# Optimization experiments

Measured on AMD Instinct MI355X. Metric: run time of the kernel, lower is better.

Reference implementation:

```python
import jax, jax.numpy as jnp
import numpy as np
from jax import lax

B, N, C = 8, 3136, 512
NUM_HEADS = 8
HEAD_DIM = C // NUM_HEADS
KS = 5  # depthwise conv kernel size


def setup_inputs() -> dict:
    key = jax.random.key(0)
    ks = jax.random.split(key, 8)
    s = 0.02
    return {
        "x": jax.random.normal(ks[0], (B, N, C), dtype=jnp.float32),
        "H": 56,
        "W": 56,
        "Wq": jax.random.normal(ks[1], (C, C), dtype=jnp.float32) * s,
        "Wkv": jax.random.normal(ks[2], (C, 2 * C), dtype=jnp.float32) * s,
        "pos_enc": jnp.zeros((1, N, C), dtype=jnp.float32),
        "dwc_w": jax.random.normal(ks[3], (HEAD_DIM, 1, KS, KS), dtype=jnp.float32) * s,
        "dwc_b": jnp.zeros((HEAD_DIM,), dtype=jnp.float32),
        "Wproj": jax.random.normal(ks[4], (C, C), dtype=jnp.float32) * s,
        "bproj": jnp.zeros((C,), dtype=jnp.float32),
    }


def _split_heads(t):
    # (B, N, C) -> (B*h, N, head_dim), matching 'b n (h c) -> (b h) n c'
    b, n, c = t.shape
    return t.reshape(b, n, NUM_HEADS, HEAD_DIM).transpose(0, 2, 1, 3).reshape(b * NUM_HEADS, n, HEAD_DIM)


def reference(x, H, W, Wq, Wkv, pos_enc, dwc_w, dwc_b, Wproj, bproj):
    b, n, c = x.shape
    # projections (qkv_bias=False)
    q = jnp.maximum(x @ Wq, 0.0)                       # ReLU kernel feature map
    kv = x @ Wkv
    k = jnp.maximum(kv[..., :c] + pos_enc, 0.0)
    v = kv[..., c:]

    q = _split_heads(q)  # (bh, n, d)
    k = _split_heads(k)
    v = _split_heads(v)

    # normalizer z_i = 1 / (q_i . sum_j k_j + eps)
    z = 1.0 / (jnp.einsum('bic,bc->bi', q, k.sum(axis=1)) + 1e-6)
    # kv-first ordering (i*j*(c+d) > c*d*(i+j) for these shapes)
    kvmat = jnp.einsum('bjc,bjd->bcd', k, v)           # (bh, d, d)
    out = jnp.einsum('bic,bcd->bid', q, kvmat) * z[..., None]

    # depthwise conv residual on v: 'b (w h) c -> b c w h'
    num = int(round(n ** 0.5))
    fmap = v.reshape(-1, num, num, HEAD_DIM).transpose(0, 3, 1, 2)  # (bh, d, num, num)
    fmap = lax.conv_general_dilated(
        fmap, dwc_w, window_strides=(1, 1), padding='SAME',
        feature_group_count=HEAD_DIM,
        dimension_numbers=('NCHW', 'OIHW', 'NCHW'))
    fmap = fmap + dwc_b[None, :, None, None]
    fmap = fmap.transpose(0, 2, 3, 1).reshape(-1, n, HEAD_DIM)
    out = out + fmap

    # merge heads: '(b h) n c -> b n (h c)'
    out = out.reshape(b, NUM_HEADS, n, HEAD_DIM).transpose(0, 2, 1, 3).reshape(b, n, c)
    return out @ Wproj + bproj
```

## Files before the change

kernel.cpp:

```cpp
#include <hip/hip_runtime.h>
#include <stdint.h>

#define B_    8
#define N_    3136
#define C_    512
#define MTOT  25088

typedef __attribute__((ext_vector_type(8))) short bf16x8;
typedef __attribute__((ext_vector_type(4))) float f32x4;

__device__ __forceinline__ float bf2f(short s){
  union { float f; uint32_t u; } cv; cv.u = ((uint32_t)(uint16_t)s) << 16; return cv.f;
}
__device__ __forceinline__ short f2bf(float f){
  union { float f; uint32_t u; } cv; cv.f = f;
  uint32_t r = cv.u + 0x7FFFu + ((cv.u >> 16) & 1u);
  return (short)(r >> 16);
}

typedef const __attribute__((address_space(1))) void* gas1_t;
typedef __attribute__((address_space(3))) void* las3_t;
__device__ __forceinline__ void gld16(const void* g, void* l){
  __builtin_amdgcn_global_load_lds((gas1_t)g, (las3_t)l, 16, 0, 0);
}

#define BARR  __builtin_amdgcn_s_barrier()
#define SCHB  __builtin_amdgcn_sched_barrier(0)
#define VMC0  asm volatile("s_waitcnt vmcnt(0)" ::: "memory")
#define VMC4  asm volatile("s_waitcnt vmcnt(4)" ::: "memory")
#define VMC6  asm volatile("s_waitcnt vmcnt(6)" ::: "memory")
#define LGKM0  asm volatile("s_waitcnt lgkmcnt(0)" ::: "memory")
#define LGKM2  asm volatile("s_waitcnt lgkmcnt(2)" ::: "memory")
#define LGKM10 asm volatile("s_waitcnt lgkmcnt(10)" ::: "memory")

__global__ __launch_bounds__(256) void cvt_x(const float* __restrict__ x,
                                             short* __restrict__ xb, int n8){
  int i = blockIdx.x * 256 + threadIdx.x;
  if (i >= n8) return;
  const float4* p = (const float4*)x;
  float4 a = p[i*2], b = p[i*2+1];
  short o[8] = { f2bf(a.x), f2bf(a.y), f2bf(a.z), f2bf(a.w),
                 f2bf(b.x), f2bf(b.y), f2bf(b.z), f2bf(b.w) };
  *(bf16x8*)(xb + i*8) = *(bf16x8*)o;
}

__global__ __launch_bounds__(256) void tconv(const float* __restrict__ src,
                                             short* __restrict__ dst, int J){
  __shared__ float tile[32][33];
  int jb = blockIdx.x * 32, kb = blockIdx.y * 32;
  int tx = threadIdx.x & 31, ty = threadIdx.x >> 5;
#pragma unroll
  for (int r = 0; r < 32; r += 8)
    tile[ty + r][tx] = src[(size_t)(kb + ty + r) * J + jb + tx];
  __syncthreads();
#pragma unroll
  for (int r = 0; r < 32; r += 8)
    dst[(size_t)(jb + ty + r) * 512 + kb + tx] = f2bf(tile[tx][ty + r]);
}

__global__ __launch_bounds__(256) void conv_wT(const float* __restrict__ w,
                                               float* __restrict__ wt){
  int i = blockIdx.x * 256 + threadIdx.x;
  if (i < 1600) { int c = i / 25, tap = i - c * 25; wt[tap * 64 + c] = w[i]; }
}

template<int MODE, int NCT>
__global__ __launch_bounds__(512, 2)
void gemm_bf16(const short* __restrict__ A, const short* __restrict__ Bt,
               short* __restrict__ oQ, short* __restrict__ oK, short* __restrict__ oV,
               const float* __restrict__ posenc,
               float* __restrict__ oF, const float* __restrict__ bias)
{
  extern __shared__ __align__(16) char lds[];
  const int tid = threadIdx.x;
  const int wave = tid >> 6, lane = tid & 63;
  const int fr = lane & 15;

  constexpr int nwg = 98 * NCT;
  constexpr int q8 = nwg / 8, r8 = nwg % 8;
  const int orig = blockIdx.x;
  const int xcd = orig & 7, lid = orig >> 3;
  const int swz = (xcd < r8 ? xcd * (q8 + 1) : r8 * (q8 + 1) + (xcd - r8) * q8) + lid;
  const int rt = (swz / NCT) * 256;
  const int ct = (swz % NCT) * 256;

  const int wm = (wave >> 2) * 128;
  const int wn = (wave & 3) * 64;

  const int srow = lane >> 2;
  const int csrc = ((lane & 3) ^ ((lane >> 3) & 3)) << 3;
  const short* srcA = A  + (size_t)(rt + wave * 32 + srow) * 512 + csrc;
  const short* srcB = Bt + (size_t)(ct + wave * 32 + srow) * 512 + csrc;
  char* dA = lds + wave * 2048;
  char* dB = lds + 32768 + wave * 2048;

  auto stage = [&](int sbb, int isB, int ks, int tt) {
    const short* s = (isB ? srcB : srcA) + tt * 64 + ks * 32;
    char* d = (isB ? dB : dA) + sbb + ks * 16384;
    gld16(s,        d);
    gld16(s + 8192, d + 1024);
  };

  const int cR   = (((lane >> 4) ^ ((fr >> 1) & 3)) << 4);
  const int offA = (wm + fr) * 64 + cR;
  const int offB = 32768 + (wn + fr) * 64 + cR;

#define READ_A(dst, bufb, ks) do { \
    const char* _p = lds + (bufb) + (ks) * 16384 + offA; \
    _Pragma("unroll") \
    for (int _i = 0; _i < 8; _i++) dst[_i] = *(const bf16x8*)(_p + _i * 1024); \
  } while (0)
#define READ_B2(dst, bufb, ks, j0) do { \
    const char* _p = lds + (bufb) + (ks) * 16384 + offB + (j0) * 1024; \
    dst[0] = *(const bf16x8*)(_p); \
    dst[1] = *(const bf16x8*)(_p + 1024); \
  } while (0)
#define MFMA16(afv, bv, jb) do { \
    __builtin_amdgcn_s_setprio(1); \
    _Pragma("unroll") \
    for (int _i = 0; _i < 8; _i++) { \
      acc[_i][jb]     = __builtin_amdgcn_mfma_f32_16x16x32_bf16(afv[_i], bv[0], acc[_i][jb],     0, 0, 0); \
      acc[_i][jb + 1] = __builtin_amdgcn_mfma_f32_16x16x32_bf16(afv[_i], bv[1], acc[_i][jb + 1], 0, 0, 0); \
    } \
    __builtin_amdgcn_s_setprio(0); \
  } while (0)

  f32x4 zv = {0.f, 0.f, 0.f, 0.f};
  f32x4 acc[8][4];
#pragma unroll
  for (int i = 0; i < 8; i++)
#pragma unroll
    for (int j = 0; j < 4; j++) acc[i][j] = zv;

  bf16x8 afU[8], afV[8], bX[2], bY[2];

  stage(0, 0, 0, 0); stage(0, 1, 0, 0); stage(0, 0, 1, 0); stage(0, 1, 1, 0);
  VMC4; BARR; SCHB;
  READ_A(afU, 0, 0);
  READ_B2(bX, 0, 0, 0);

  for (int t = 0; t < 7; ++t) {
    const int bufb = (t & 1) * 65536, sbb = bufb ^ 65536;
    stage(sbb, 0, 0, t + 1);
    VMC6; BARR; SCHB;
    READ_B2(bY, bufb, 0, 2);
    LGKM2; SCHB;
    MFMA16(afU, bX, 0);
    stage(sbb, 1, 0, t + 1);
    VMC4; BARR; SCHB;
    READ_A(afV, bufb, 1);
    READ_B2(bX, bufb, 1, 0);
    LGKM10; SCHB;
    MFMA16(afU, bY, 2);
    stage(sbb, 0, 1, t + 1);
    VMC6; BARR; SCHB;
    READ_B2(bY, bufb, 1, 2);
    LGKM2; SCHB;
    MFMA16(afV, bX, 0);
    stage(sbb, 1, 1, t + 1);
    VMC4; BARR; SCHB;
    READ_A(afU, sbb, 0);
    READ_B2(bX, sbb, 0, 0);
    LGKM10; SCHB;
    MFMA16(afV, bY, 2);
  }
  {
    const int bufb = 65536;
    VMC4; BARR; SCHB;
    READ_B2(bY, bufb, 0, 2);
    LGKM2; SCHB;
    MFMA16(afU, bX, 0);
    VMC0; BARR; SCHB;
    READ_A(afV, bufb, 1);
    READ_B2(bX, bufb, 1, 0);
    LGKM10; SCHB;
    MFMA16(afU, bY, 2);
    READ_B2(bY, bufb, 1, 2);
    LGKM2; SCHB;
    MFMA16(afV, bX, 0);
    LGKM0; SCHB;
    MFMA16(afV, bY, 2);
  }

  BARR; SCHB;

  const int rb = (lane >> 4) << 2;
  if (MODE == 0) {
    short* ov = (short*)lds;
    const int sel = ct >> 9;
    const int cb  = ct - sel * 512;
    short* outp = sel == 0 ? oQ : (sel == 1 ? oK : oV);
#pragma unroll
    for (int q4 = 0; q4 < 4; ++q4) {
      if (q4) __syncthreads();
      if ((wave >> 2) == (q4 >> 1)) {
        const int ib = (q4 & 1) * 4;
#pragma unroll
        for (int ii = 0; ii < 4; ii++)
#pragma unroll
          for (int j = 0; j < 4; j++)
#pragma unroll
            for (int r = 0; r < 4; r++)
              ov[(ii * 16 + rb + r) * 260 + wn + j * 16 + fr] = f2bf(acc[ib + ii][j][r]);
      }
      __syncthreads();
#pragma unroll
      for (int p = 0; p < 4; ++p) {
        int id = tid + 512 * p;
        int row = id >> 5, cc = (id & 31) * 8;
        bf16x8 vv = *(const bf16x8*)&ov[row * 260 + cc];
        int grow = rt + q4 * 64 + row;
        short o[8];
        if (sel == 0) {
#pragma unroll
          for (int e = 0; e < 8; e++) o[e] = f2bf(fmaxf(bf2f(vv[e]), 0.f));
        } else if (sel == 1) {
          int nr = grow % N_;
          const float* pp = posenc + (size_t)nr * 512 + cb + cc;
          f32x4 p0 = *(const f32x4*)pp;
          f32x4 p1 = *(const f32x4*)(pp + 4);
#pragma unroll
          for (int e = 0; e < 4; e++) {
            o[e]     = f2bf(fmaxf(bf2f(vv[e]) + p0[e], 0.f));
            o[e + 4] = f2bf(fmaxf(bf2f(vv[e + 4]) + p1[e], 0.f));
          }
        } else {
#pragma unroll
          for (int e = 0; e < 8; e++) o[e] = vv[e];
        }
        *(bf16x8*)(outp + (size_t)grow * 512 + cb + cc) = *(bf16x8*)o;
      }
    }
  } else {
    float* ovf = (float*)lds;
#pragma unroll
    for (int q4 = 0; q4 < 4; ++q4) {
      if (q4) __syncthreads();
      if ((wave >> 2) == (q4 >> 1)) {
        const int ib = (q4 & 1) * 4;
#pragma unroll
        for (int ii = 0; ii < 4; ii++)
#pragma unroll
          for (int j = 0; j < 4; j++)
#pragma unroll
            for (int r = 0; r < 4; r++)
              ovf[(ii * 16 + rb + r) * 260 + wn + j * 16 + fr] = acc[ib + ii][j][r];
      }
      __syncthreads();
#pragma unroll
      for (int p = 0; p < 4; ++p) {
        int id = tid + 512 * p;
        int row = id >> 5, cc = (id & 31) * 8;
        f32x4 v0 = *(const f32x4*)&ovf[row * 260 + cc];
        f32x4 v1 = *(const f32x4*)&ovf[row * 260 + cc + 4];
        v0 += *(const f32x4*)&bias[ct + cc];
        v1 += *(const f32x4*)&bias[ct + cc + 4];
        float* op = oF + (size_t)(rt + q4 * 64 + row) * 512 + ct + cc;
        *(f32x4*)op       = v0;
        *(f32x4*)(op + 4) = v1;
      }
    }
  }
#undef READ_A
#undef READ_B2
#undef MFMA16
}

__global__ __launch_bounds__(256)
void kvmat_part(const short* __restrict__ kb, const short* __restrict__ vb,
                float* __restrict__ pKV, float* __restrict__ pKS)
{
  __shared__ __align__(16) float lk[64][64];
  __shared__ __align__(16) float lv[64][64];
  const int chunk = blockIdx.x, bh = blockIdx.y;
  const int b = bh >> 3, h = bh & 7;
  const int t = threadIdx.x;
  const int tc = t >> 4, td = t & 15;
  const int kc = t & 63, kr = (t >> 6) * 16;
  float acc[4][4] = {};
  float ksacc = 0.f;

  for (int tile = 0; tile < 7; ++tile) {
    const int r0 = chunk * 448 + tile * 64;
    __syncthreads();
#pragma unroll
    for (int i = 0; i < 2; i++) {
      int idx = t + i * 256;
      int r = idx >> 3, c8 = (idx & 7) << 3;
      size_t g = (size_t)(b * N_ + r0 + r) * 512 + h * 64 + c8;
      bf16x8 kk = *(const bf16x8*)(kb + g);
      bf16x8 vv = *(const bf16x8*)(vb + g);
#pragma unroll
      for (int e = 0; e < 8; e++) { lk[r][c8 + e] = bf2f(kk[e]); lv[r][c8 + e] = bf2f(vv[e]); }
    }
    __syncthreads();
#pragma unroll 4
    for (int r = 0; r < 64; r++) {
      f32x4 k4 = *(const f32x4*)&lk[r][tc * 4];
      f32x4 v4 = *(const f32x4*)&lv[r][td * 4];
#pragma unroll
      for (int i = 0; i < 4; i++)
#pragma unroll
        for (int j = 0; j < 4; j++) acc[i][j] += k4[i] * v4[j];
    }
#pragma unroll 4
    for (int rr = 0; rr < 16; rr++) ksacc += lk[kr + rr][kc];
  }

  const int pbase = (bh * 7 + chunk) * 4096;
#pragma unroll
  for (int i = 0; i < 4; i++)
#pragma unroll
    for (int j = 0; j < 4; j++)
      pKV[pbase + (tc * 4 + i) * 64 + td * 4 + j] = acc[i][j];
  __syncthreads();
  float* red = &lk[0][0];
  red[t] = ksacc;
  __syncthreads();
  if (t < 64)
    pKS[(bh * 7 + chunk) * 64 + t] = red[t] + red[t + 64] + red[t + 128] + red[t + 192];
}

__global__ __launch_bounds__(256)
void kv_reduce(const float* __restrict__ pKV, const float* __restrict__ pKS,
               short* __restrict__ kvT, float* __restrict__ ksum)
{
  int bh = blockIdx.x, t = threadIdx.x;
#pragma unroll
  for (int i = 0; i < 16; i++) {
    int idx = t + i * 256;
    float s = 0.f;
#pragma unroll
    for (int c = 0; c < 7; c++) s += pKV[(bh * 7 + c) * 4096 + idx];
    int cc = idx >> 6, d = idx & 63;
    kvT[bh * 4096 + d * 64 + cc] = f2bf(s);
  }
  if (t < 64) {
    float s = 0.f;
#pragma unroll
    for (int c = 0; c < 7; c++) s += pKS[(bh * 7 + c) * 64 + t];
    ksum[bh * 64 + t] = s;
  }
}

__global__ __launch_bounds__(256)
void conv_dw(const short* __restrict__ vb, const float* __restrict__ wT,
             const float* __restrict__ bias, short* __restrict__ pre)
{
  __shared__ __align__(16) short lsv[5 * 56 * 64];
  __shared__ __align__(16) float lwT[25 * 64];
  const int y = blockIdx.x, bh = blockIdx.y;
  const int b = bh >> 3, h = bh & 7;
  const int t = threadIdx.x;
  for (int i = t; i < 1600; i += 256) lwT[i] = wT[i];
  for (int i = t; i < 2240; i += 256) {
    int row = i / 448, rem = i - row * 448;
    int xx = rem >> 3, c8i = rem & 7;
    int gy = y + row - 2;
    bf16x8 val = {0, 0, 0, 0, 0, 0, 0, 0};
    if ((unsigned)gy < 56u)
      val = *(const bf16x8*)(vb + (size_t)(b * N_ + gy * 56 + xx) * 512 + h * 64 + c8i * 8);
    *(bf16x8*)(lsv + i * 8) = val;
  }
  __syncthreads();

  const int c8 = t & 7;
  const int x0 = t >> 3;
  float acc0[8], acc1[8];
  {
    f32x4 b0 = *(const f32x4*)&bias[c8 * 8];
    f32x4 b1 = *(const f32x4*)&bias[c8 * 8 + 4];
#pragma unroll
    for (int e = 0; e < 4; e++) { acc0[e] = b0[e]; acc0[e+4] = b1[e];
                                  acc1[e] = b0[e]; acc1[e+4] = b1[e]; }
  }
#pragma unroll
  for (int dy = 0; dy < 5; ++dy) {
#pragma unroll
    for (int dx = 0; dx < 5; ++dx) {
      float w8[8];
      {
        const float* wp = &lwT[(dy * 5 + dx) * 64 + c8 * 8];
        *(f32x4*)&w8[0] = *(const f32x4*)wp;
        *(f32x4*)&w8[4] = *(const f32x4*)(wp + 4);
      }
      const int base = dy * 56 * 64 + c8 * 8;
      int xxa = x0 + dx - 2;
      if ((unsigned)xxa < 56u) {
        bf16x8 v = *(const bf16x8*)(lsv + base + xxa * 64);
#pragma unroll
        for (int e = 0; e < 8; e++) acc0[e] += bf2f(v[e]) * w8[e];
      }
      int xxb = xxa + 32;
      if (xxb < 56) {
        bf16x8 v = *(const bf16x8*)(lsv + base + xxb * 64);
#pragma unroll
        for (int e = 0; e < 8; e++) acc1[e] += bf2f(v[e]) * w8[e];
      }
    }
  }
  size_t gbase = (size_t)(b * N_ + y * 56 + x0) * 512 + h * 64 + c8 * 8;
  short o[8];
#pragma unroll
  for (int e = 0; e < 8; e++) o[e] = f2bf(acc0[e]);
  *(bf16x8*)(pre + gbase) = *(bf16x8*)o;
  if (x0 + 32 < 56) {
#pragma unroll
    for (int e = 0; e < 8; e++) o[e] = f2bf(acc1[e]);
    *(bf16x8*)(pre + gbase + (size_t)32 * 512) = *(bf16x8*)o;
  }
}

__global__ __launch_bounds__(64)
void attn_mfma(const short* __restrict__ qb, const short* __restrict__ kvT,
               const float* __restrict__ ksum, short* __restrict__ pre)
{
  __shared__ __align__(16) float ov[64 * 68];
  __shared__ float lks[64];
  const int pt = blockIdx.x, bh = blockIdx.y;
  const int b = bh >> 3, h = bh & 7;
  const int l = threadIdx.x;
  const int fr = l & 15, kg = l >> 4;
  const int n0 = pt * 64;

  lks[l] = ksum[bh * 64 + l];

  const short* qbase = qb + (size_t)(b * N_ + n0) * 512 + h * 64;
  const short* kvb   = kvT + bh * 4096;
  bf16x8 af[4][2], bm[4][2];
#pragma unroll
  for (int i = 0; i < 4; i++)
#pragma unroll
    for (int s = 0; s < 2; s++) {
      af[i][s] = *(const bf16x8*)(qbase + (size_t)(fr + i * 16) * 512 + s * 32 + kg * 8);
      bm[i][s] = *(const bf16x8*)(kvb + (fr + i * 16) * 64 + s * 32 + kg * 8);
    }

  f32x4 zv4 = {0.f, 0.f, 0.f, 0.f};
  f32x4 acc[4][4];
#pragma unroll
  for (int i = 0; i < 4; i++)
#pragma unroll
    for (int j = 0; j < 4; j++) acc[i][j] = zv4;
#pragma unroll
  for (int s = 0; s < 2; s++)
#pragma unroll
    for (int i = 0; i < 4; i++)
#pragma unroll
      for (int j = 0; j < 4; j++)
        acc[i][j] = __builtin_amdgcn_mfma_f32_16x16x32_bf16(af[i][s], bm[j][s], acc[i][j], 0, 0, 0);

  const short* qrow = qb + (size_t)(b * N_ + n0 + l) * 512 + h * 64;
  float zd = 0.f;
#pragma unroll
  for (int g = 0; g < 8; g++) {
    bf16x8 qv = *(const bf16x8*)(qrow + g * 8);
#pragma unroll
    for (int e = 0; e < 8; e++) zd += bf2f(qv[e]) * lks[g * 8 + e];
  }
  const float z = 1.f / (zd + 1e-6f);

  const int rb = kg << 2;
#pragma unroll
  for (int i = 0; i < 4; i++)
#pragma unroll
    for (int j = 0; j < 4; j++)
#pragma unroll
      for (int r = 0; r < 4; r++)
        ov[(i * 16 + rb + r) * 68 + j * 16 + fr] = acc[i][j][r];
  __syncthreads();

  size_t gb = (size_t)(b * N_ + n0 + l) * 512 + h * 64;
  const float* ovr = &ov[l * 68];
#pragma unroll
  for (int g = 0; g < 8; g++) {
    bf16x8 pv = *(const bf16x8*)(pre + gb + g * 8);
    f32x4 a0 = *(const f32x4*)(ovr + g * 8);
    f32x4 a1 = *(const f32x4*)(ovr + g * 8 + 4);
    short o[8];
#pragma unroll
    for (int e = 0; e < 4; e++) {
      o[e]     = f2bf(a0[e] * z + bf2f(pv[e]));
      o[e + 4] = f2bf(a1[e] * z + bf2f(pv[e + 4]));
    }
    *(bf16x8*)(pre + gb + g * 8) = *(bf16x8*)o;
  }
}

extern "C" void kernel_launch(void* const* d_in, const int* in_sizes, int n_in,
                              void* d_out, int out_size, void* d_ws, size_t ws_size,
                              hipStream_t stream)
{
  const float* x     = (const float*)d_in[0];
  const float* Wq    = (const float*)d_in[3];
  const float* Wkv   = (const float*)d_in[4];
  const float* pos   = (const float*)d_in[5];
  const float* dwcw  = (const float*)d_in[6];
  const float* dwcb  = (const float*)d_in[7];
  const float* Wproj = (const float*)d_in[8];
  const float* bproj = (const float*)d_in[9];
  float* out = (float*)d_out;

  char* ws = (char*)d_ws;
  size_t off = 0;
  auto alloc = [&](size_t bytes) -> void* {
    void* p = ws + off;
    off = (off + bytes + 255) & ~(size_t)255;
    return p;
  };
  short* xb     = (short*)alloc((size_t)MTOT * 512 * 2);
  short* wqkvT  = (short*)alloc((size_t)1536 * 512 * 2);
  short* wprojT = (short*)alloc((size_t)512 * 512 * 2);
  float* wTc    = (float*)alloc((size_t)25 * 64 * 4);
  short* qb     = (short*)alloc((size_t)MTOT * 512 * 2);
  short* kbuf   = (short*)alloc((size_t)MTOT * 512 * 2);
  short* vbuf   = (short*)alloc((size_t)MTOT * 512 * 2);
  float* pKV    = (float*)alloc((size_t)64 * 7 * 4096 * 4);
  float* pKS    = (float*)alloc((size_t)64 * 7 * 64 * 4);
  short* kvT    = (short*)alloc((size_t)64 * 4096 * 2);
  float* ksumB  = (float*)alloc((size_t)64 * 64 * 4);
  short* pre    = (short*)alloc((size_t)MTOT * 512 * 2);
  if (ws_size < off) return;

  {
    auto k0 = gemm_bf16<0, 6>;
    auto k1 = gemm_bf16<1, 2>;
    hipFuncSetAttribute(reinterpret_cast<const void*>(k0),
                        hipFuncAttributeMaxDynamicSharedMemorySize, 131072);
    hipFuncSetAttribute(reinterpret_cast<const void*>(k1),
                        hipFuncAttributeMaxDynamicSharedMemorySize, 131072);
  }

  cvt_x<<<dim3((MTOT * 512 / 8 + 255) / 256), dim3(256), 0, stream>>>(x, xb, MTOT * 512 / 8);
  conv_wT<<<dim3(7), dim3(256), 0, stream>>>(dwcw, wTc);
  tconv<<<dim3(16, 16), dim3(256), 0, stream>>>(Wq,    wqkvT,              512);
  tconv<<<dim3(32, 16), dim3(256), 0, stream>>>(Wkv,   wqkvT + 512 * 512, 1024);
  tconv<<<dim3(16, 16), dim3(256), 0, stream>>>(Wproj, wprojT,             512);
  gemm_bf16<0, 6><<<dim3(588), dim3(512), 131072, stream>>>(xb, wqkvT, qb, kbuf, vbuf, pos,
                                                            nullptr, nullptr);
  kvmat_part<<<dim3(7, 64), dim3(256), 0, stream>>>(kbuf, vbuf, pKV, pKS);
  kv_reduce<<<dim3(64), dim3(256), 0, stream>>>(pKV, pKS, kvT, ksumB);
  conv_dw<<<dim3(56, 64), dim3(256), 0, stream>>>(vbuf, wTc, dwcb, pre);
  attn_mfma<<<dim3(49, 64), dim3(64), 0, stream>>>(qb, kvT, ksumB, pre);
  gemm_bf16<1, 2><<<dim3(196), dim3(512), 131072, stream>>>(pre, wprojT, nullptr, nullptr, nullptr,
                                                            nullptr, out, bproj);
}
```

Measured before the change: 220.5 us.

## Shrink GEMM tiles and use a three-stage LDS pipeline for higher occupancy

Rewrites the bf16 GEMM mainloop to use 128-row tiles (128x256 for the QKV projection, 128x128 for the output projection) with a simple three-buffer, K-step-of-32 pipeline in place of the hand-scheduled double-buffered 256x256 loop. LDS usage and register footprint drop so launch bounds rise to 4 blocks per CU, and the grids quadruple or double. The epilogue becomes a single LDS staging pass. The aim is more workgroups to fill the CUs and more latency hiding from occupancy. The cost is lower per-block data reuse, more global traffic for the operands, and the loss of the interleaved LDS-read/MFMA scheduling.

```diff
diff --git a/kernel.cpp b/kernel.cpp
--- a/kernel.cpp
+++ b/kernel.cpp
@@ -27,11 +27,9 @@
 #define BARR  __builtin_amdgcn_s_barrier()
 #define SCHB  __builtin_amdgcn_sched_barrier(0)
 #define VMC0  asm volatile("s_waitcnt vmcnt(0)" ::: "memory")
-#define VMC4  asm volatile("s_waitcnt vmcnt(4)" ::: "memory")
-#define VMC6  asm volatile("s_waitcnt vmcnt(6)" ::: "memory")
-#define LGKM0  asm volatile("s_waitcnt lgkmcnt(0)" ::: "memory")
-#define LGKM2  asm volatile("s_waitcnt lgkmcnt(2)" ::: "memory")
-#define LGKM10 asm volatile("s_waitcnt lgkmcnt(10)" ::: "memory")
+#define VMC2  asm volatile("s_waitcnt vmcnt(2)" ::: "memory")
+#define VMC3  asm volatile("s_waitcnt vmcnt(3)" ::: "memory")
+#define LGKM0 asm volatile("s_waitcnt lgkmcnt(0)" ::: "memory")
 
 __global__ __launch_bounds__(256) void cvt_x(const float* __restrict__ x,
                                              short* __restrict__ xb, int n8){
@@ -65,121 +63,82 @@
 }
 
 template<int MODE, int NCT>
-__global__ __launch_bounds__(512, 2)
+__global__ __launch_bounds__(512, 4)
 void gemm_bf16(const short* __restrict__ A, const short* __restrict__ Bt,
                short* __restrict__ oQ, short* __restrict__ oK, short* __restrict__ oV,
                const float* __restrict__ posenc,
                float* __restrict__ oF, const float* __restrict__ bias)
 {
+  constexpr int BN    = MODE ? 128 : 256;
+  constexpr int NJ    = MODE ? 2 : 4;
+  constexpr int WNW   = MODE ? 32 : 64;
+  constexpr int BUFSZ = MODE ? 16384 : 24576;
+  constexpr int BOFF  = 8192;
   extern __shared__ __align__(16) char lds[];
   const int tid = threadIdx.x;
   const int wave = tid >> 6, lane = tid & 63;
   const int fr = lane & 15;
 
-  constexpr int nwg = 98 * NCT;
+  constexpr int nwg = 196 * NCT;
   constexpr int q8 = nwg / 8, r8 = nwg % 8;
   const int orig = blockIdx.x;
   const int xcd = orig & 7, lid = orig >> 3;
   const int swz = (xcd < r8 ? xcd * (q8 + 1) : r8 * (q8 + 1) + (xcd - r8) * q8) + lid;
-  const int rt = (swz / NCT) * 256;
-  const int ct = (swz % NCT) * 256;
-
-  const int wm = (wave >> 2) * 128;
-  const int wn = (wave & 3) * 64;
+  const int rt = (swz / NCT) * 128;
+  const int ct = (swz % NCT) * BN;
+
+  const int wm = (wave >> 2) * 64;
+  const int wn = (wave & 3) * WNW;
 
   const int srow = lane >> 2;
   const int csrc = ((lane & 3) ^ ((lane >> 3) & 3)) << 3;
-  const short* srcA = A  + (size_t)(rt + wave * 32 + srow) * 512 + csrc;
-  const short* srcB = Bt + (size_t)(ct + wave * 32 + srow) * 512 + csrc;
-  char* dA = lds + wave * 2048;
-  char* dB = lds + 32768 + wave * 2048;
-
-  auto stage = [&](int sbb, int isB, int ks, int tt) {
-    const short* s = (isB ? srcB : srcA) + tt * 64 + ks * 32;
-    char* d = (isB ? dB : dA) + sbb + ks * 16384;
-    gld16(s,        d);
-    gld16(s + 8192, d + 1024);
+  const short* srcA = A  + (size_t)(rt + wave * 16 + srow) * 512 + csrc;
+  const short* srcB = Bt + (size_t)(ct + wave * (MODE ? 16 : 32) + srow) * 512 + csrc;
+  char* dA = lds + wave * 1024;
+  char* dB = lds + BOFF + wave * (MODE ? 1024 : 2048);
+
+  auto stage = [&](int t) {
+    const int b = (t % 3) * BUFSZ;
+    const short* a0 = srcA + t * 32;
+    gld16(a0, dA + b);
+    const short* b0 = srcB + t * 32;
+    gld16(b0, dB + b);
+    if (MODE == 0) gld16(b0 + 8192, dB + b + 1024);
   };
 
   const int cR   = (((lane >> 4) ^ ((fr >> 1) & 3)) << 4);
   const int offA = (wm + fr) * 64 + cR;
-  const int offB = 32768 + (wn + fr) * 64 + cR;
-
-#define READ_A(dst, bufb, ks) do { \
-    const char* _p = lds + (bufb) + (ks) * 16384 + offA; \
-    _Pragma("unroll") \
-    for (int _i = 0; _i < 8; _i++) dst[_i] = *(const bf16x8*)(_p + _i * 1024); \
-  } while (0)
-#define READ_B2(dst, bufb, ks, j0) do { \
-    const char* _p = lds + (bufb) + (ks) * 16384 + offB + (j0) * 1024; \
-    dst[0] = *(const bf16x8*)(_p); \
-    dst[1] = *(const bf16x8*)(_p + 1024); \
-  } while (0)
-#define MFMA16(afv, bv, jb) do { \
-    __builtin_amdgcn_s_setprio(1); \
-    _Pragma("unroll") \
-    for (int _i = 0; _i < 8; _i++) { \
-      acc[_i][jb]     = __builtin_amdgcn_mfma_f32_16x16x32_bf16(afv[_i], bv[0], acc[_i][jb],     0, 0, 0); \
-      acc[_i][jb + 1] = __builtin_amdgcn_mfma_f32_16x16x32_bf16(afv[_i], bv[1], acc[_i][jb + 1], 0, 0, 0); \
-    } \
-    __builtin_amdgcn_s_setprio(0); \
-  } while (0)
+  const int offB = BOFF + (wn + fr) * 64 + cR;
 
   f32x4 zv = {0.f, 0.f, 0.f, 0.f};
-  f32x4 acc[8][4];
-#pragma unroll
-  for (int i = 0; i < 8; i++)
-#pragma unroll
-    for (int j = 0; j < 4; j++) acc[i][j] = zv;
-
-  bf16x8 afU[8], afV[8], bX[2], bY[2];
-
-  stage(0, 0, 0, 0); stage(0, 1, 0, 0); stage(0, 0, 1, 0); stage(0, 1, 1, 0);
-  VMC4; BARR; SCHB;
-  READ_A(afU, 0, 0);
-  READ_B2(bX, 0, 0, 0);
-
-  for (int t = 0; t < 7; ++t) {
-    const int bufb = (t & 1) * 65536, sbb = bufb ^ 65536;
-    stage(sbb, 0, 0, t + 1);
-    VMC6; BARR; SCHB;
-    READ_B2(bY, bufb, 0, 2);
-    LGKM2; SCHB;
-    MFMA16(afU, bX, 0);
-    stage(sbb, 1, 0, t + 1);
-    VMC4; BARR; SCHB;
-    READ_A(afV, bufb, 1);
-    READ_B2(bX, bufb, 1, 0);
-    LGKM10; SCHB;
-    MFMA16(afU, bY, 2);
-    stage(sbb, 0, 1, t + 1);
-    VMC6; BARR; SCHB;
-    READ_B2(bY, bufb, 1, 2);
-    LGKM2; SCHB;
-    MFMA16(afV, bX, 0);
-    stage(sbb, 1, 1, t + 1);
-    VMC4; BARR; SCHB;
-    READ_A(afU, sbb, 0);
-    READ_B2(bX, sbb, 0, 0);
-    LGKM10; SCHB;
-    MFMA16(afV, bY, 2);
-  }
-  {
-    const int bufb = 65536;
-    VMC4; BARR; SCHB;
-    READ_B2(bY, bufb, 0, 2);
-    LGKM2; SCHB;
-    MFMA16(afU, bX, 0);
-    VMC0; BARR; SCHB;
-    READ_A(afV, bufb, 1);
-    READ_B2(bX, bufb, 1, 0);
-    LGKM10; SCHB;
-    MFMA16(afU, bY, 2);
-    READ_B2(bY, bufb, 1, 2);
-    LGKM2; SCHB;
-    MFMA16(afV, bX, 0);
+  f32x4 acc[4][NJ];
+#pragma unroll
+  for (int i = 0; i < 4; i++)
+#pragma unroll
+    for (int j = 0; j < NJ; j++) acc[i][j] = zv;
+
+  stage(0); stage(1);
+
+#pragma unroll
+  for (int t = 0; t < 16; ++t) {
+    if (t < 15) { if (MODE == 0) { VMC3; } else { VMC2; } }
+    else       { VMC0; }
+    BARR; SCHB;
+    if (t + 2 < 16) stage(t + 2);
+    const char* sb = lds + (t % 3) * BUFSZ;
+    bf16x8 af[4], bfr[NJ];
+#pragma unroll
+    for (int i = 0; i < 4; i++) af[i] = *(const bf16x8*)(sb + offA + i * 1024);
+#pragma unroll
+    for (int j = 0; j < NJ; j++) bfr[j] = *(const bf16x8*)(sb + offB + j * 1024);
     LGKM0; SCHB;
-    MFMA16(afV, bY, 2);
+    __builtin_amdgcn_s_setprio(1);
+#pragma unroll
+    for (int i = 0; i < 4; i++)
+#pragma unroll
+      for (int j = 0; j < NJ; j++)
+        acc[i][j] = __builtin_amdgcn_mfma_f32_16x16x32_bf16(af[i], bfr[j], acc[i][j], 0, 0, 0);
+    __builtin_amdgcn_s_setprio(0);
   }
 
   BARR; SCHB;
@@ -191,79 +150,62 @@
     const int cb  = ct - sel * 512;
     short* outp = sel == 0 ? oQ : (sel == 1 ? oK : oV);
 #pragma unroll
-    for (int q4 = 0; q4 < 4; ++q4) {
-      if (q4) __syncthreads();
-      if ((wave >> 2) == (q4 >> 1)) {
-        const int ib = (q4 & 1) * 4;
-#pragma unroll
-        for (int ii = 0; ii < 4; ii++)
-#pragma unroll
-          for (int j = 0; j < 4; j++)
-#pragma unroll
-            for (int r = 0; r < 4; r++)
-              ov[(ii * 16 + rb + r) * 260 + wn + j * 16 + fr] = f2bf(acc[ib + ii][j][r]);
+    for (int i = 0; i < 4; i++)
+#pragma unroll
+      for (int j = 0; j < 4; j++)
+#pragma unroll
+        for (int r = 0; r < 4; r++)
+          ov[(wm + i * 16 + rb + r) * 264 + wn + j * 16 + fr] = f2bf(acc[i][j][r]);
+    __syncthreads();
+#pragma unroll
+    for (int p = 0; p < 8; ++p) {
+      int id = tid + 512 * p;
+      int row = id >> 5, cc = (id & 31) * 8;
+      bf16x8 vv = *(const bf16x8*)&ov[row * 264 + cc];
+      int grow = rt + row;
+      short o[8];
+      if (sel == 0) {
+#pragma unroll
+        for (int e = 0; e < 8; e++) o[e] = f2bf(fmaxf(bf2f(vv[e]), 0.f));
+      } else if (sel == 1) {
+        int nr = grow % N_;
+        const float* pp = posenc + (size_t)nr * 512 + cb + cc;
+        f32x4 p0 = *(const f32x4*)pp;
+        f32x4 p1 = *(const f32x4*)(pp + 4);
+#pragma unroll
+        for (int e = 0; e < 4; e++) {
+          o[e]     = f2bf(fmaxf(bf2f(vv[e]) + p0[e], 0.f));
+          o[e + 4] = f2bf(fmaxf(bf2f(vv[e + 4]) + p1[e], 0.f));
+        }
+      } else {
+#pragma unroll
+        for (int e = 0; e < 8; e++) o[e] = vv[e];
       }
-      __syncthreads();
-#pragma unroll
-      for (int p = 0; p < 4; ++p) {
-        int id = tid + 512 * p;
-        int row = id >> 5, cc = (id & 31) * 8;
-        bf16x8 vv = *(const bf16x8*)&ov[row * 260 + cc];
-        int grow = rt + q4 * 64 + row;
-        short o[8];
-        if (sel == 0) {
-#pragma unroll
-          for (int e = 0; e < 8; e++) o[e] = f2bf(fmaxf(bf2f(vv[e]), 0.f));
-        } else if (sel == 1) {
-          int nr = grow % N_;
-          const float* pp = posenc + (size_t)nr * 512 + cb + cc;
-          f32x4 p0 = *(const f32x4*)pp;
-          f32x4 p1 = *(const f32x4*)(pp + 4);
-#pragma unroll
-          for (int e = 0; e < 4; e++) {
-            o[e]     = f2bf(fmaxf(bf2f(vv[e]) + p0[e], 0.f));
-            o[e + 4] = f2bf(fmaxf(bf2f(vv[e + 4]) + p1[e], 0.f));
-          }
-        } else {
-#pragma unroll
-          for (int e = 0; e < 8; e++) o[e] = vv[e];
-        }
-        *(bf16x8*)(outp + (size_t)grow * 512 + cb + cc) = *(bf16x8*)o;
-      }
+      *(bf16x8*)(outp + (size_t)grow * 512 + cb + cc) = *(bf16x8*)o;
     }
   } else {
     float* ovf = (float*)lds;
 #pragma unroll
-    for (int q4 = 0; q4 < 4; ++q4) {
-      if (q4) __syncthreads();
-      if ((wave >> 2) == (q4 >> 1)) {
-        const int ib = (q4 & 1) * 4;
-#pragma unroll
-        for (int ii = 0; ii < 4; ii++)
-#pragma unroll
-          for (int j = 0; j < 4; j++)
-#pragma unroll
-            for (int r = 0; r < 4; r++)
-              ovf[(ii * 16 + rb + r) * 260 + wn + j * 16 + fr] = acc[ib + ii][j][r];
-      }
-      __syncthreads();
-#pragma unroll
-      for (int p = 0; p < 4; ++p) {
-        int id = tid + 512 * p;
-        int row = id >> 5, cc = (id & 31) * 8;
-        f32x4 v0 = *(const f32x4*)&ovf[row * 260 + cc];
-        f32x4 v1 = *(const f32x4*)&ovf[row * 260 + cc + 4];
-        v0 += *(const f32x4*)&bias[ct + cc];
-        v1 += *(const f32x4*)&bias[ct + cc + 4];
-        float* op = oF + (size_t)(rt + q4 * 64 + row) * 512 + ct + cc;
-        *(f32x4*)op       = v0;
-        *(f32x4*)(op + 4) = v1;
-      }
-    }
-  }
-#undef READ_A
-#undef READ_B2
-#undef MFMA16
+    for (int i = 0; i < 4; i++)
+#pragma unroll
+      for (int j = 0; j < 2; j++)
+#pragma unroll
+        for (int r = 0; r < 4; r++)
+          ovf[(wm + i * 16 + rb + r) * 132 + wn + j * 16 + fr] = acc[i][j][r];
+    __syncthreads();
+#pragma unroll
+    for (int p = 0; p < 4; ++p) {
+      int id = tid + 512 * p;
+      int row = id >> 4, cc = (id & 15) * 8;
+      f32x4 v0 = *(const f32x4*)&ovf[row * 132 + cc];
+      f32x4 v1 = *(const f32x4*)&ovf[row * 132 + cc + 4];
+      v0 += *(const f32x4*)&bias[ct + cc];
+      v1 += *(const f32x4*)&bias[ct + cc + 4];
+      float* op = oF + (size_t)(rt + row) * 512 + ct + cc;
+      *(f32x4*)op       = v0;
+      *(f32x4*)(op + 4) = v1;
+    }
+  }
 }
 
 __global__ __launch_bounds__(256)
@@ -524,11 +466,11 @@
 
   {
     auto k0 = gemm_bf16<0, 6>;
-    auto k1 = gemm_bf16<1, 2>;
+    auto k1 = gemm_bf16<1, 4>;
     hipFuncSetAttribute(reinterpret_cast<const void*>(k0),
-                        hipFuncAttributeMaxDynamicSharedMemorySize, 131072);
+                        hipFuncAttributeMaxDynamicSharedMemorySize, 73728);
     hipFuncSetAttribute(reinterpret_cast<const void*>(k1),
-                        hipFuncAttributeMaxDynamicSharedMemorySize, 131072);
+                        hipFuncAttributeMaxDynamicSharedMemorySize, 67584);
   }
 
   cvt_x<<<dim3((MTOT * 512 / 8 + 255) / 256), dim3(256), 0, stream>>>(x, xb, MTOT * 512 / 8);
@@ -536,12 +478,12 @@
   tconv<<<dim3(16, 16), dim3(256), 0, stream>>>(Wq,    wqkvT,              512);
   tconv<<<dim3(32, 16), dim3(256), 0, stream>>>(Wkv,   wqkvT + 512 * 512, 1024);
   tconv<<<dim3(16, 16), dim3(256), 0, stream>>>(Wproj, wprojT,             512);
-  gemm_bf16<0, 6><<<dim3(588), dim3(512), 131072, stream>>>(xb, wqkvT, qb, kbuf, vbuf, pos,
+  gemm_bf16<0, 6><<<dim3(1176), dim3(512), 73728, stream>>>(xb, wqkvT, qb, kbuf, vbuf, pos,
                                                             nullptr, nullptr);
   kvmat_part<<<dim3(7, 64), dim3(256), 0, stream>>>(kbuf, vbuf, pKV, pKS);
   kv_reduce<<<dim3(64), dim3(256), 0, stream>>>(pKV, pKS, kvT, ksumB);
   conv_dw<<<dim3(56, 64), dim3(256), 0, stream>>>(vbuf, wTc, dwcb, pre);
   attn_mfma<<<dim3(49, 64), dim3(64), 0, stream>>>(qb, kvT, ksumB, pre);
-  gemm_bf16<1, 2><<<dim3(196), dim3(512), 131072, stream>>>(pre, wprojT, nullptr, nullptr, nullptr,
-                                                            nullptr, out, bproj);
-}
+  gemm_bf16<1, 4><<<dim3(784), dim3(512), 67584, stream>>>(pre, wprojT, nullptr, nullptr, nullptr,
+                                                           nullptr, out, bproj);
+}
```

Measured after the change: 216.1 us. -2.0%, faster.
